# Kernel optimization log

Measured on AMD Instinct MI355X. Metric: run time of the kernel, lower is better.

Reference implementation:

```python
import jax, jax.numpy as jnp
import numpy as np

NUM_TOKENS = 8192
DIM = 256
BETA = 0.25
DECAY = 0.99
EPS = 1e-05


def setup_inputs() -> dict:
    key = jax.random.key(0)
    k1, k2 = jax.random.split(key, 2)
    z = jax.random.normal(k1, (16, DIM, 32, 32), dtype=jnp.float32)
    embedding = jax.random.normal(k2, (NUM_TOKENS, DIM), dtype=jnp.float32)
    cluster_size = jnp.zeros((NUM_TOKENS,), dtype=jnp.float32)
    ema_w = embedding  # module init copies embed_init into both embedding and ema_w
    return {"z": z, "embedding": embedding, "cluster_size": cluster_size, "ema_w": ema_w}


def reference(z, embedding, cluster_size, ema_w):
    # z: [B, D, H, W] -> [B, H, W, D]
    zp = jnp.transpose(z, (0, 2, 3, 1))
    zf = zp.reshape(-1, DIM)  # [N, D]
    # squared euclidean distances [N, K] via ||z||^2 + ||e||^2 - 2 z.e
    d = (jnp.sum(zf * zf, axis=1, keepdims=True)
         + jnp.sum(embedding * embedding, axis=1)
         - 2.0 * (zf @ embedding.T))
    idx = jnp.argmin(d, axis=1)  # [N]
    z_q = embedding[idx].reshape(zp.shape)  # [B, H, W, D]

    # training-mode EMA statistics (pure-functional: returned as new states)
    counts = jax.ops.segment_sum(jnp.ones(zf.shape[0], dtype=zf.dtype), idx,
                                 num_segments=NUM_TOKENS)
    embed_sum = jax.ops.segment_sum(zf, idx, num_segments=NUM_TOKENS)  # [K, D]
    cs = cluster_size * DECAY + (1.0 - DECAY) * counts
    new_ema_w = ema_w * DECAY + (1.0 - DECAY) * embed_sum
    # torch evaluates sum AFTER add_(eps): denom = sum(cs + eps) + K*eps
    cs = cs + EPS
    new_cluster_size = cs / (jnp.sum(cs) + NUM_TOKENS * EPS)
    new_embedding = new_ema_w / new_cluster_size[:, None]

    loss = BETA * jnp.mean((jax.lax.stop_gradient(z_q) - zp) ** 2)
    # straight-through estimator
    z_q_st = zp + jax.lax.stop_gradient(z_q - zp)
    out = jnp.transpose(z_q_st, (0, 3, 1, 2))  # back to [B, D, H, W]
    return out, loss, idx, new_cluster_size, new_ema_w, new_embedding
```

## Files before the change

kernel.cpp:

```cpp
#include <hip/hip_runtime.h>

#define N_TOK   16384
#define K_CODES 8192
#define DIMS    256

#define OUT_OFF  0
#define LOSS_OFF 4194304
#define IDX_OFF  4194305
#define NCS_OFF  4210689
#define NEMA_OFF 4218881
#define NEMB_OFF 6316033

#define WS_ZFRAG  0u
#define WS_EFRAG  16777216u
#define WS_ENORM  25165824u
#define WS_PVAL   25198592u
#define WS_PIDX   25460736u
#define WS_IDXI   25722880u
#define WS_CNT    25788416u
#define WS_CS     25821184u
#define WS_OFFS   25853952u
#define WS_WPOS   25886720u
#define WS_TLIST  25919488u
#define WS_DENOM  25985024u

typedef _Float16 f16x8 __attribute__((ext_vector_type(8)));
typedef float    f32x16 __attribute__((ext_vector_type(16)));

union HU { _Float16 h; unsigned short u; };

static __device__ inline void split_f32(float x, unsigned short& hi, unsigned short& lo) {
    HU a; a.h = (_Float16)x;
    float r = (x - (float)a.h) * 2048.0f;
    HU b; b.h = (_Float16)r;
    hi = a.u; lo = b.u;
}

static __device__ inline float join_f16(unsigned short h, unsigned short l) {
    HU a, b; a.u = h; b.u = l;
    return (float)a.h + (float)b.h * 4.8828125e-4f;
}

#define GLD16(gp, lp) __builtin_amdgcn_global_load_lds( \
    (const __attribute__((address_space(1))) unsigned int*)(gp), \
    (__attribute__((address_space(3))) unsigned int*)(lp), 16, 0, 0)

__global__ __launch_bounds__(256) void cvt_z_kernel(const float* __restrict__ z,
                                                    unsigned short* __restrict__ zfrag,
                                                    float* __restrict__ loss_cell,
                                                    double* __restrict__ denom) {
    __shared__ float T[64][65];
    const int t = threadIdx.x;
    const int hg = blockIdx.x & 15, dg = (blockIdx.x >> 4) & 3, b = blockIdx.x >> 6;
    if (blockIdx.x == 0 && t == 0) { *loss_cell = 0.f; *denom = 0.0; }
    const int c4 = (t & 15) * 4, r0 = t >> 4;
    const float* zb = z + (((size_t)(b * 256 + dg * 64)) << 10) + hg * 64;
#pragma unroll
    for (int p = 0; p < 4; ++p) {
        const int r = r0 + p * 16;
        const float4 v = *(const float4*)(zb + ((size_t)r << 10) + c4);
        T[r][c4] = v.x; T[r][c4 + 1] = v.y; T[r][c4 + 2] = v.z; T[r][c4 + 3] = v.w;
    }
    __syncthreads();
    const int tr = t & 63, dc = (t >> 6) * 16;
    const int tile = b * 16 + hg;
    const int tg = tile * 2 + (tr >> 5), l31 = tr & 31;
    const int ks = dg * 4 + (dc >> 4);
    unsigned short hb[16], lb[16];
#pragma unroll
    for (int j = 0; j < 16; ++j) split_f32(T[dc + j][tr], hb[j], lb[j]);
#pragma unroll
    for (int lv = 0; lv < 2; ++lv) {
        const unsigned short* src = lv ? lb : hb;
        unsigned short* dst = zfrag + (size_t)((tg * 2 + lv) * 16 + ks) * 512;
        *(uint4*)(dst + l31 * 8)       = ((const uint4*)src)[0];
        *(uint4*)(dst + 256 + l31 * 8) = ((const uint4*)src)[1];
    }
}

__global__ __launch_bounds__(256) void cvt_e_enorm(const float* __restrict__ emb,
                                                   unsigned short* __restrict__ efrag,
                                                   float* __restrict__ enorm,
                                                   int* __restrict__ cnt) {
    __shared__ double red[256];
    const int t = threadIdx.x, g = blockIdx.x;
    const int lane = t & 63, q = t >> 6;
    const int l31 = lane & 31, lhi = lane >> 5;
    if (g < 32) cnt[g * 256 + t] = 0;
    const float* rowp = emb + (size_t)(g * 32 + l31) * 256 + lhi * 8;
    double s = 0.0;
#pragma unroll
    for (int kk = 0; kk < 4; ++kk) {
        const int ks = q * 4 + kk;
        const float4 a = *(const float4*)(rowp + ks * 16);
        const float4 bq = *(const float4*)(rowp + ks * 16 + 4);
        const float vv[8] = {a.x, a.y, a.z, a.w, bq.x, bq.y, bq.z, bq.w};
        unsigned short hb[8], lb[8];
#pragma unroll
        for (int j = 0; j < 8; ++j) {
            split_f32(vv[j], hb[j], lb[j]);
            s += (double)vv[j] * (double)vv[j];
        }
        *(uint4*)(efrag + (size_t)((g * 2 + 0) * 16 + ks) * 512 + lane * 8) = *(const uint4*)hb;
        *(uint4*)(efrag + (size_t)((g * 2 + 1) * 16 + ks) * 512 + lane * 8) = *(const uint4*)lb;
    }
    red[t] = s;
    __syncthreads();
    if (t < 32) {
        double acc = 0.0;
#pragma unroll
        for (int qq = 0; qq < 4; ++qq) acc += red[qq * 64 + t] + red[qq * 64 + 32 + t];
        enorm[g * 32 + t] = (float)acc;
    }
}

__global__ __launch_bounds__(256, 2) void argmin_mfma(
    const unsigned short* __restrict__ zfrag, const unsigned short* __restrict__ efrag,
    const float* __restrict__ enorm, float* __restrict__ pval, int* __restrict__ pidx) {
    __shared__ __align__(16) unsigned short E[2][8192];
    __shared__ float en_s[2][64];

    const int tid = threadIdx.x, lane = tid & 63, wave = tid >> 6;
    const int tile = blockIdx.x & 127, csplit = blockIdx.x >> 7;
    const int token0 = tile * 128, code0 = csplit * 2048;

    f16x8 Zr[2][16];
    {
        const unsigned short* zb = zfrag + (size_t)(tile * 4 + wave) * 16384 + lane * 8;
#pragma unroll
        for (int lv = 0; lv < 2; ++lv)
#pragma unroll
            for (int ks = 0; ks < 16; ++ks)
                Zr[lv][ks] = *(const f16x8*)(zb + (lv * 16 + ks) * 512);
    }

    const int slv = wave >> 1, scg = wave & 1;

    float bv = 3.4e38f; int bi = 0;

#pragma unroll
    for (int ksl = 0; ksl < 4; ++ksl) {
        const unsigned short* sp = efrag +
            (size_t)(((csplit * 64 + scg) * 2 + slv) * 16 + ksl) * 512 + lane * 8;
        GLD16(sp, &E[0][(wave * 4 + ksl) * 512]);
    }
    if (tid < 64) en_s[0][tid] = enorm[code0 + tid];
    __syncthreads();

    for (int ct = 0; ct < 32; ++ct) {
        f32x16 acc_h[2], acc_l[2];
#pragma unroll
        for (int cg = 0; cg < 2; ++cg)
#pragma unroll
            for (int qq = 0; qq < 16; ++qq) { acc_h[cg][qq] = 0.f; acc_l[cg][qq] = 0.f; }

#pragma unroll
        for (int kc = 0; kc < 4; ++kc) {
            const int p = (ct * 4 + kc) & 1;
            if (!(ct == 31 && kc == 3)) {
                const int nch = ct * 4 + kc + 1;
                const int nct = nch >> 2, nkc = nch & 3;
                const int g = csplit * 64 + nct * 2 + scg;
#pragma unroll
                for (int ksl = 0; ksl < 4; ++ksl) {
                    const unsigned short* sp = efrag +
                        (size_t)((g * 2 + slv) * 16 + nkc * 4 + ksl) * 512 + lane * 8;
                    GLD16(sp, &E[p ^ 1][(wave * 4 + ksl) * 512]);
                }
            }
            if (kc == 0 && ct < 31 && tid < 64)
                en_s[(ct + 1) & 1][tid] = enorm[code0 + (ct + 1) * 64 + tid];

#pragma unroll
            for (int ksl = 0; ksl < 4; ++ksl) {
                const int ks = kc * 4 + ksl;
                f16x8 ae[2][2];
#pragma unroll
                for (int lv = 0; lv < 2; ++lv)
#pragma unroll
                    for (int cg = 0; cg < 2; ++cg)
                        ae[lv][cg] = *(const f16x8*)&E[p][((lv * 2 + cg) * 4 + ksl) * 512 + lane * 8];
#pragma unroll
                for (int cg = 0; cg < 2; ++cg) {
                    acc_h[cg] = __builtin_amdgcn_mfma_f32_32x32x16_f16(ae[0][cg], Zr[0][ks], acc_h[cg], 0, 0, 0);
                    acc_l[cg] = __builtin_amdgcn_mfma_f32_32x32x16_f16(ae[0][cg], Zr[1][ks], acc_l[cg], 0, 0, 0);
                    acc_l[cg] = __builtin_amdgcn_mfma_f32_32x32x16_f16(ae[1][cg], Zr[0][ks], acc_l[cg], 0, 0, 0);
                }
            }
            if (kc == 3) {
                const int rbase = 4 * (lane >> 5);
#pragma unroll
                for (int cg = 0; cg < 2; ++cg)
#pragma unroll
                    for (int r = 0; r < 16; ++r) {
                        const int cl = cg * 32 + (r & 3) + 8 * (r >> 2) + rbase;
                        const float s = en_s[ct & 1][cl] -
                            2.0f * (acc_h[cg][r] + acc_l[cg][r] * 4.8828125e-4f);
                        const int code = code0 + ct * 64 + cl;
                        if (s < bv) { bv = s; bi = code; }
                    }
            }
            __syncthreads();
        }
    }
    {
        const float ov = __shfl_xor(bv, 32);
        const int   oi = __shfl_xor(bi, 32);
        if (ov < bv || (ov == bv && oi < bi)) { bv = ov; bi = oi; }
    }
    if (lane < 32) {
        const int n = token0 + wave * 32 + lane;
        pval[csplit * N_TOK + n] = bv;
        pidx[csplit * N_TOK + n] = bi;
    }
}

__global__ __launch_bounds__(256) void combine4_kernel(
    const float* __restrict__ pval, const int* __restrict__ pidx,
    int* __restrict__ idx_i, float* __restrict__ idx_f, int* __restrict__ cnt) {
    const int n = blockIdx.x * 256 + threadIdx.x;
    float bv = pval[n]; int bi = pidx[n];
#pragma unroll
    for (int s = 1; s < 4; ++s) {
        const float v = pval[s * N_TOK + n];
        const int i = pidx[s * N_TOK + n];
        if (v < bv || (v == bv && i < bi)) { bv = v; bi = i; }
    }
    idx_i[n] = bi;
    idx_f[n] = (float)bi;
    atomicAdd(&cnt[bi], 1);
}

__global__ __launch_bounds__(256) void scan_kernel(const int* __restrict__ cnt,
                                                   int* __restrict__ offs,
                                                   int* __restrict__ wpos) {
    __shared__ int part[256];
    const int tid = threadIdx.x;
    const int base = tid * 32;
    int loc[32];
    int s = 0;
#pragma unroll
    for (int j = 0; j < 32; ++j) { loc[j] = cnt[base + j]; s += loc[j]; }
    part[tid] = s;
    __syncthreads();
    for (int off = 1; off < 256; off <<= 1) {
        int v = 0;
        if (tid >= off) v = part[tid - off];
        __syncthreads();
        if (tid >= off) part[tid] += v;
        __syncthreads();
    }
    int run = (tid > 0) ? part[tid - 1] : 0;
#pragma unroll
    for (int j = 0; j < 32; ++j) {
        offs[base + j] = run;
        wpos[base + j] = run;
        run += loc[j];
    }
}

__global__ __launch_bounds__(256) void scatter_cs(
    const int* __restrict__ idx_i, int* __restrict__ wpos, int* __restrict__ tlist,
    const float* __restrict__ cluster_size, const int* __restrict__ cnt,
    float* __restrict__ cs, double* __restrict__ denom) {
    __shared__ double red[256];
    const int t = threadIdx.x, b = blockIdx.x;
    if (b < 64) {
        const int n = b * 256 + t;
        const int k = idx_i[n];
        tlist[atomicAdd(&wpos[k], 1)] = n;
    } else {
        const int k = (b - 64) * 256 + t;
        const float v = cluster_size[k] * 0.99f + 0.01f * (float)cnt[k] + 1e-5f;
        cs[k] = v;
        red[t] = (double)v;
        __syncthreads();
        for (int s2 = 128; s2; s2 >>= 1) {
            if (t < s2) red[t] += red[t + s2];
            __syncthreads();
        }
        if (t == 0) atomicAdd(denom, red[0]);
    }
}

__global__ __launch_bounds__(256) void nema_gather(
    const unsigned short* __restrict__ zfrag,
    const int* __restrict__ offs, const int* __restrict__ cnt, const int* __restrict__ tlist,
    const float* __restrict__ ema_w, const float* __restrict__ cs,
    const double* __restrict__ denom, float* __restrict__ ncs_out,
    float* __restrict__ nema_out, float* __restrict__ nemb_out,
    const float* __restrict__ z, const float* __restrict__ emb,
    const int* __restrict__ idx_i, float* __restrict__ out, float* __restrict__ loss_cell) {
    __shared__ float redf[256];
    const int t = threadIdx.x;
    if (blockIdx.x < 2048) {
        const int lane = t & 63, wave = t >> 6;
        const int k = blockIdx.x * 4 + wave;
        const int l31 = lane & 31, sel = lane >> 5;
        const int beg = offs[k], c = cnt[k];
        float acc[8] = {0.f, 0.f, 0.f, 0.f, 0.f, 0.f, 0.f, 0.f};
        for (int i = 0; i < c; ++i) {
            const int tok = tlist[beg + i];
            const int tg = tok >> 5, tl = tok & 31;
            const uint4 v = *(const uint4*)(zfrag +
                (size_t)((tg * 2 + sel) * 16 + (l31 >> 1)) * 512 + (l31 & 1) * 256 + tl * 8);
            uint4 o;
            o.x = __shfl_xor((int)v.x, 32); o.y = __shfl_xor((int)v.y, 32);
            o.z = __shfl_xor((int)v.z, 32); o.w = __shfl_xor((int)v.w, 32);
            if (lane < 32) {
                const unsigned short* hp = (const unsigned short*)&v;
                const unsigned short* lp = (const unsigned short*)&o;
#pragma unroll
                for (int j = 0; j < 8; ++j) acc[j] += join_f16(hp[j], lp[j]);
            }
        }
        const float dn = (float)(*denom) + (float)K_CODES * 1e-5f;
        const float ncs = cs[k] / dn;
        if (lane == 0) ncs_out[k] = ncs;
        if (lane < 32) {
            const size_t off = ((size_t)k << 8) + l31 * 8;
#pragma unroll
            for (int j = 0; j < 8; ++j) {
                const float ne = ema_w[off + j] * 0.99f + 0.01f * acc[j];
                nema_out[off + j] = ne;
                nemb_out[off + j] = ne / ncs;
            }
        }
    } else {
        const int gb = blockIdx.x - 2048;
        const int n0 = (gb >> 2) * 64;
        const int dg = (gb & 3) * 64;
        const int b = n0 >> 10, hw0 = n0 & 1023;
        const int lane = t & 63, w = t >> 6;
        const int n = n0 + lane;
        const int k = idx_i[n];
        const float* zb = z + ((size_t)b << 18) + hw0 + lane;
        float* ob = out + ((size_t)b << 18) + hw0 + lane;
        float ls = 0.f;
#pragma unroll 4
        for (int d = dg + w; d < dg + 64; d += 4) {
            const float zv = zb[(size_t)d << 10];
            const float ev = emb[((size_t)k << 8) + d];
            ob[(size_t)d << 10] = ev;
            const float df = ev - zv;
            ls += df * df;
        }
        redf[t] = ls;
        __syncthreads();
        for (int s2 = 128; s2; s2 >>= 1) {
            if (t < s2) redf[t] += redf[t + s2];
            __syncthreads();
        }
        if (t == 0) atomicAdd(loss_cell, redf[0] * (0.25f / 4194304.0f));
    }
}

extern "C" void kernel_launch(void* const* d_in, const int* in_sizes, int n_in,
                              void* d_out, int out_size, void* d_ws, size_t ws_size,
                              hipStream_t stream) {
    const float* z            = (const float*)d_in[0];
    const float* emb          = (const float*)d_in[1];
    const float* cluster_size = (const float*)d_in[2];
    const float* ema_w        = (const float*)d_in[3];
    float* out = (float*)d_out;
    char*  wsb = (char*)d_ws;

    unsigned short* zfrag = (unsigned short*)(wsb + WS_ZFRAG);
    unsigned short* efrag = (unsigned short*)(wsb + WS_EFRAG);
    float*  enorm  = (float*)(wsb + WS_ENORM);
    float*  pval   = (float*)(wsb + WS_PVAL);
    int*    pidx   = (int*)(wsb + WS_PIDX);
    int*    idx_i  = (int*)(wsb + WS_IDXI);
    int*    cnt    = (int*)(wsb + WS_CNT);
    float*  cs     = (float*)(wsb + WS_CS);
    int*    offs   = (int*)(wsb + WS_OFFS);
    int*    wpos   = (int*)(wsb + WS_WPOS);
    int*    tlist  = (int*)(wsb + WS_TLIST);
    double* denom  = (double*)(wsb + WS_DENOM);

    cvt_z_kernel<<<1024, 256, 0, stream>>>(z, zfrag, out + LOSS_OFF, denom);
    cvt_e_enorm<<<256, 256, 0, stream>>>(emb, efrag, enorm, cnt);
    argmin_mfma<<<512, 256, 0, stream>>>(zfrag, efrag, enorm, pval, pidx);
    combine4_kernel<<<N_TOK / 256, 256, 0, stream>>>(pval, pidx, idx_i,
                                                     out + IDX_OFF, cnt);
    scan_kernel<<<1, 256, 0, stream>>>(cnt, offs, wpos);
    scatter_cs<<<96, 256, 0, stream>>>(idx_i, wpos, tlist, cluster_size, cnt, cs, denom);
    nema_gather<<<3072, 256, 0, stream>>>(zfrag, offs, cnt, tlist, ema_w, cs, denom,
                                          out + NCS_OFF, out + NEMA_OFF, out + NEMB_OFF,
                                          z, emb, idx_i, out + OUT_OFF, out + LOSS_OFF);
}
```

Measured before the change: 424.6 us.

## Deepen argmin E-tile pipeline to four LDS stages with explicit vmcnt waits

The argmin MFMA kernel moves from a double-buffered E tile to a four-slot LDS ring with a prefetch distance of two chunks. Each step now waits with a partial s_waitcnt vmcnt, so later chunks can still be in flight, and uses a single raw s_barrier instead of a trailing __syncthreads. The kernel also preloads all 2048 code norms into LDS once at the start, and raises wave priority around the MFMA block. The aim is to hide global-to-LDS latency and cut barrier stalls, at the cost of more LDS per block (about 72KB), which could limit occupancy, and fragile hand-counted vmcnt values.

```diff
diff --git a/kernel.cpp b/kernel.cpp
--- a/kernel.cpp
+++ b/kernel.cpp
@@ -117,8 +117,8 @@
 __global__ __launch_bounds__(256, 2) void argmin_mfma(
     const unsigned short* __restrict__ zfrag, const unsigned short* __restrict__ efrag,
     const float* __restrict__ enorm, float* __restrict__ pval, int* __restrict__ pidx) {
-    __shared__ __align__(16) unsigned short E[2][8192];
-    __shared__ float en_s[2][64];
+    __shared__ __align__(16) unsigned short E[4][8192];
+    __shared__ __align__(16) float en_all[2048];
 
     const int tid = threadIdx.x, lane = tid & 63, wave = tid >> 6;
     const int tile = blockIdx.x & 127, csplit = blockIdx.x >> 7;
@@ -136,16 +136,26 @@
 
     const int slv = wave >> 1, scg = wave & 1;
 
+    auto stage = [&](int ch) {
+        const int g = csplit * 64 + (ch >> 2) * 2 + scg;
+        const int nkc = ch & 3;
+#pragma unroll
+        for (int ksl = 0; ksl < 4; ++ksl) {
+            const unsigned short* sp = efrag +
+                (size_t)((g * 2 + slv) * 16 + nkc * 4 + ksl) * 512 + lane * 8;
+            GLD16(sp, &E[ch & 3][(wave * 4 + ksl) * 512]);
+        }
+    };
+
+#pragma unroll
+    for (int c = 0; c < 2; ++c) {
+        const float* sp = enorm + code0 + (wave * 2 + c) * 256 + lane * 4;
+        GLD16(sp, &en_all[(wave * 2 + c) * 256]);
+    }
+    stage(0);
+    stage(1);
+
     float bv = 3.4e38f; int bi = 0;
-
-#pragma unroll
-    for (int ksl = 0; ksl < 4; ++ksl) {
-        const unsigned short* sp = efrag +
-            (size_t)(((csplit * 64 + scg) * 2 + slv) * 16 + ksl) * 512 + lane * 8;
-        GLD16(sp, &E[0][(wave * 4 + ksl) * 512]);
-    }
-    if (tid < 64) en_s[0][tid] = enorm[code0 + tid];
-    __syncthreads();
 
     for (int ct = 0; ct < 32; ++ct) {
         f32x16 acc_h[2], acc_l[2];
@@ -156,21 +166,21 @@
 
 #pragma unroll
         for (int kc = 0; kc < 4; ++kc) {
-            const int p = (ct * 4 + kc) & 1;
-            if (!(ct == 31 && kc == 3)) {
-                const int nch = ct * 4 + kc + 1;
-                const int nct = nch >> 2, nkc = nch & 3;
-                const int g = csplit * 64 + nct * 2 + scg;
-#pragma unroll
-                for (int ksl = 0; ksl < 4; ++ksl) {
-                    const unsigned short* sp = efrag +
-                        (size_t)((g * 2 + slv) * 16 + nkc * 4 + ksl) * 512 + lane * 8;
-                    GLD16(sp, &E[p ^ 1][(wave * 4 + ksl) * 512]);
-                }
+            if (kc <= 1) {
+                stage(ct * 4 + kc + 2);
+                asm volatile("s_waitcnt vmcnt(8)" ::: "memory");
+            } else if (ct < 31) {
+                stage(ct * 4 + kc + 2);
+                asm volatile("s_waitcnt vmcnt(8)" ::: "memory");
+            } else if (kc == 2) {
+                asm volatile("s_waitcnt vmcnt(4)" ::: "memory");
+            } else {
+                asm volatile("s_waitcnt vmcnt(0)" ::: "memory");
             }
-            if (kc == 0 && ct < 31 && tid < 64)
-                en_s[(ct + 1) & 1][tid] = enorm[code0 + (ct + 1) * 64 + tid];
-
+            __builtin_amdgcn_s_barrier();
+            __builtin_amdgcn_sched_barrier(0);
+
+            __builtin_amdgcn_s_setprio(1);
 #pragma unroll
             for (int ksl = 0; ksl < 4; ++ksl) {
                 const int ks = kc * 4 + ksl;
@@ -179,7 +189,7 @@
                 for (int lv = 0; lv < 2; ++lv)
 #pragma unroll
                     for (int cg = 0; cg < 2; ++cg)
-                        ae[lv][cg] = *(const f16x8*)&E[p][((lv * 2 + cg) * 4 + ksl) * 512 + lane * 8];
+                        ae[lv][cg] = *(const f16x8*)&E[kc][((lv * 2 + cg) * 4 + ksl) * 512 + lane * 8];
 #pragma unroll
                 for (int cg = 0; cg < 2; ++cg) {
                     acc_h[cg] = __builtin_amdgcn_mfma_f32_32x32x16_f16(ae[0][cg], Zr[0][ks], acc_h[cg], 0, 0, 0);
@@ -187,6 +197,8 @@
                     acc_l[cg] = __builtin_amdgcn_mfma_f32_32x32x16_f16(ae[1][cg], Zr[0][ks], acc_l[cg], 0, 0, 0);
                 }
             }
+            __builtin_amdgcn_s_setprio(0);
+
             if (kc == 3) {
                 const int rbase = 4 * (lane >> 5);
 #pragma unroll
@@ -194,13 +206,12 @@
 #pragma unroll
                     for (int r = 0; r < 16; ++r) {
                         const int cl = cg * 32 + (r & 3) + 8 * (r >> 2) + rbase;
-                        const float s = en_s[ct & 1][cl] -
+                        const float s = en_all[ct * 64 + cl] -
                             2.0f * (acc_h[cg][r] + acc_l[cg][r] * 4.8828125e-4f);
                         const int code = code0 + ct * 64 + cl;
                         if (s < bv) { bv = s; bi = code; }
                     }
             }
-            __syncthreads();
         }
     }
     {
```

Result: no change. 425.9 us (+0.3%).

## Double per-wave token tile in argmin MFMA kernel to reuse codebook loads

Applied to the files above, without the earlier changes.

Each wave now keeps two 32-token Z fragment sets in registers and reuses every codebook fragment staged in LDS for both, so each block covers 256 tokens and half as many blocks are launched. Codebook traffic from global memory and LDS per token is halved. All 2048 codebook norms for the block's split are loaded once into LDS up front, replacing the per-tile reload. In exchange, register use roughly doubles, occupancy drops to one block per CU, and only 256 blocks run, which may leave some compute units underused.

```diff
diff --git a/kernel.cpp b/kernel.cpp
--- a/kernel.cpp
+++ b/kernel.cpp
@@ -114,62 +114,69 @@
     }
 }
 
-__global__ __launch_bounds__(256, 2) void argmin_mfma(
+__global__ __launch_bounds__(256, 1) void argmin_mfma(
     const unsigned short* __restrict__ zfrag, const unsigned short* __restrict__ efrag,
     const float* __restrict__ enorm, float* __restrict__ pval, int* __restrict__ pidx) {
     __shared__ __align__(16) unsigned short E[2][8192];
-    __shared__ float en_s[2][64];
+    __shared__ __align__(16) float en_all[2048];
 
     const int tid = threadIdx.x, lane = tid & 63, wave = tid >> 6;
-    const int tile = blockIdx.x & 127, csplit = blockIdx.x >> 7;
-    const int token0 = tile * 128, code0 = csplit * 2048;
-
-    f16x8 Zr[2][16];
+    const int csplit = blockIdx.x & 3;
+    const int tile   = blockIdx.x >> 2;
+    const int token0 = tile * 256, code0 = csplit * 2048;
+
+    f16x8 Zr[2][2][16];
     {
-        const unsigned short* zb = zfrag + (size_t)(tile * 4 + wave) * 16384 + lane * 8;
-#pragma unroll
-        for (int lv = 0; lv < 2; ++lv)
-#pragma unroll
-            for (int ks = 0; ks < 16; ++ks)
-                Zr[lv][ks] = *(const f16x8*)(zb + (lv * 16 + ks) * 512);
+        const int tgbase = tile * 8 + wave * 2;
+#pragma unroll
+        for (int tg = 0; tg < 2; ++tg) {
+            const unsigned short* zb = zfrag + (size_t)(tgbase + tg) * 16384 + lane * 8;
+#pragma unroll
+            for (int lv = 0; lv < 2; ++lv)
+#pragma unroll
+                for (int ks = 0; ks < 16; ++ks)
+                    Zr[tg][lv][ks] = *(const f16x8*)(zb + (lv * 16 + ks) * 512);
+        }
     }
 
     const int slv = wave >> 1, scg = wave & 1;
 
-    float bv = 3.4e38f; int bi = 0;
-
-#pragma unroll
-    for (int ksl = 0; ksl < 4; ++ksl) {
-        const unsigned short* sp = efrag +
-            (size_t)(((csplit * 64 + scg) * 2 + slv) * 16 + ksl) * 512 + lane * 8;
-        GLD16(sp, &E[0][(wave * 4 + ksl) * 512]);
-    }
-    if (tid < 64) en_s[0][tid] = enorm[code0 + tid];
+    auto stage = [&](int ph) {
+        const int g = csplit * 64 + (ph >> 2) * 2 + scg;
+        const int nkc = ph & 3;
+#pragma unroll
+        for (int ksl = 0; ksl < 4; ++ksl) {
+            const unsigned short* sp = efrag +
+                (size_t)((g * 2 + slv) * 16 + nkc * 4 + ksl) * 512 + lane * 8;
+            GLD16(sp, &E[ph & 1][(wave * 4 + ksl) * 512]);
+        }
+    };
+
+#pragma unroll
+    for (int c = 0; c < 2; ++c) {
+        const float* sp = enorm + code0 + (wave * 2 + c) * 256 + lane * 4;
+        GLD16(sp, &en_all[(wave * 2 + c) * 256]);
+    }
+    stage(0);
     __syncthreads();
 
+    float bv[2] = {3.4e38f, 3.4e38f};
+    int   bi[2] = {0, 0};
+
     for (int ct = 0; ct < 32; ++ct) {
-        f32x16 acc_h[2], acc_l[2];
-#pragma unroll
-        for (int cg = 0; cg < 2; ++cg)
-#pragma unroll
-            for (int qq = 0; qq < 16; ++qq) { acc_h[cg][qq] = 0.f; acc_l[cg][qq] = 0.f; }
+        f32x16 acc_h[2][2], acc_l[2][2];
+#pragma unroll
+        for (int tg = 0; tg < 2; ++tg)
+#pragma unroll
+            for (int cg = 0; cg < 2; ++cg)
+#pragma unroll
+                for (int qq = 0; qq < 16; ++qq) {
+                    acc_h[tg][cg][qq] = 0.f; acc_l[tg][cg][qq] = 0.f;
+                }
 
 #pragma unroll
         for (int kc = 0; kc < 4; ++kc) {
-            const int p = (ct * 4 + kc) & 1;
-            if (!(ct == 31 && kc == 3)) {
-                const int nch = ct * 4 + kc + 1;
-                const int nct = nch >> 2, nkc = nch & 3;
-                const int g = csplit * 64 + nct * 2 + scg;
-#pragma unroll
-                for (int ksl = 0; ksl < 4; ++ksl) {
-                    const unsigned short* sp = efrag +
-                        (size_t)((g * 2 + slv) * 16 + nkc * 4 + ksl) * 512 + lane * 8;
-                    GLD16(sp, &E[p ^ 1][(wave * 4 + ksl) * 512]);
-                }
-            }
-            if (kc == 0 && ct < 31 && tid < 64)
-                en_s[(ct + 1) & 1][tid] = enorm[code0 + (ct + 1) * 64 + tid];
+            if (!(ct == 31 && kc == 3)) stage(ct * 4 + kc + 1);
 
 #pragma unroll
             for (int ksl = 0; ksl < 4; ++ksl) {
@@ -179,39 +186,52 @@
                 for (int lv = 0; lv < 2; ++lv)
 #pragma unroll
                     for (int cg = 0; cg < 2; ++cg)
-                        ae[lv][cg] = *(const f16x8*)&E[p][((lv * 2 + cg) * 4 + ksl) * 512 + lane * 8];
-#pragma unroll
-                for (int cg = 0; cg < 2; ++cg) {
-                    acc_h[cg] = __builtin_amdgcn_mfma_f32_32x32x16_f16(ae[0][cg], Zr[0][ks], acc_h[cg], 0, 0, 0);
-                    acc_l[cg] = __builtin_amdgcn_mfma_f32_32x32x16_f16(ae[0][cg], Zr[1][ks], acc_l[cg], 0, 0, 0);
-                    acc_l[cg] = __builtin_amdgcn_mfma_f32_32x32x16_f16(ae[1][cg], Zr[0][ks], acc_l[cg], 0, 0, 0);
-                }
+                        ae[lv][cg] = *(const f16x8*)&E[kc & 1][((lv * 2 + cg) * 4 + ksl) * 512 + lane * 8];
+#pragma unroll
+                for (int tg = 0; tg < 2; ++tg)
+#pragma unroll
+                    for (int cg = 0; cg < 2; ++cg)
+                        acc_h[tg][cg] = __builtin_amdgcn_mfma_f32_32x32x16_f16(ae[0][cg], Zr[tg][0][ks], acc_h[tg][cg], 0, 0, 0);
+#pragma unroll
+                for (int tg = 0; tg < 2; ++tg)
+#pragma unroll
+                    for (int cg = 0; cg < 2; ++cg)
+                        acc_l[tg][cg] = __builtin_amdgcn_mfma_f32_32x32x16_f16(ae[0][cg], Zr[tg][1][ks], acc_l[tg][cg], 0, 0, 0);
+#pragma unroll
+                for (int tg = 0; tg < 2; ++tg)
+#pragma unroll
+                    for (int cg = 0; cg < 2; ++cg)
+                        acc_l[tg][cg] = __builtin_amdgcn_mfma_f32_32x32x16_f16(ae[1][cg], Zr[tg][0][ks], acc_l[tg][cg], 0, 0, 0);
             }
+
             if (kc == 3) {
                 const int rbase = 4 * (lane >> 5);
 #pragma unroll
-                for (int cg = 0; cg < 2; ++cg)
-#pragma unroll
-                    for (int r = 0; r < 16; ++r) {
-                        const int cl = cg * 32 + (r & 3) + 8 * (r >> 2) + rbase;
-                        const float s = en_s[ct & 1][cl] -
-                            2.0f * (acc_h[cg][r] + acc_l[cg][r] * 4.8828125e-4f);
-                        const int code = code0 + ct * 64 + cl;
-                        if (s < bv) { bv = s; bi = code; }
-                    }
+                for (int tg = 0; tg < 2; ++tg)
+#pragma unroll
+                    for (int cg = 0; cg < 2; ++cg)
+#pragma unroll
+                        for (int r = 0; r < 16; ++r) {
+                            const int cl = cg * 32 + (r & 3) + 8 * (r >> 2) + rbase;
+                            const float s = en_all[ct * 64 + cl] -
+                                2.0f * (acc_h[tg][cg][r] + acc_l[tg][cg][r] * 4.8828125e-4f);
+                            const int code = code0 + ct * 64 + cl;
+                            if (s < bv[tg]) { bv[tg] = s; bi[tg] = code; }
+                        }
             }
             __syncthreads();
         }
     }
-    {
-        const float ov = __shfl_xor(bv, 32);
-        const int   oi = __shfl_xor(bi, 32);
-        if (ov < bv || (ov == bv && oi < bi)) { bv = ov; bi = oi; }
-    }
-    if (lane < 32) {
-        const int n = token0 + wave * 32 + lane;
-        pval[csplit * N_TOK + n] = bv;
-        pidx[csplit * N_TOK + n] = bi;
+#pragma unroll
+    for (int tg = 0; tg < 2; ++tg) {
+        const float ov = __shfl_xor(bv[tg], 32);
+        const int   oi = __shfl_xor(bi[tg], 32);
+        if (ov < bv[tg] || (ov == bv[tg] && oi < bi[tg])) { bv[tg] = ov; bi[tg] = oi; }
+        if (lane < 32) {
+            const int n = token0 + wave * 64 + tg * 32 + lane;
+            pval[csplit * N_TOK + n] = bv[tg];
+            pidx[csplit * N_TOK + n] = bi[tg];
+        }
     }
 }
 
@@ -380,7 +400,7 @@
 
     cvt_z_kernel<<<1024, 256, 0, stream>>>(z, zfrag, out + LOSS_OFF, denom);
     cvt_e_enorm<<<256, 256, 0, stream>>>(emb, efrag, enorm, cnt);
-    argmin_mfma<<<512, 256, 0, stream>>>(zfrag, efrag, enorm, pval, pidx);
+    argmin_mfma<<<256, 256, 0, stream>>>(zfrag, efrag, enorm, pval, pidx);
     combine4_kernel<<<N_TOK / 256, 256, 0, stream>>>(pval, pidx, idx_i,
                                                      out + IDX_OFF, cnt);
     scan_kernel<<<1, 256, 0, stream>>>(cnt, offs, wpos);
```

After: 436.0 us. 1.03x slower.
